# Optimization experiments

Measured on AMD Instinct MI355X. Metric: run time of the kernel, lower is better.

The kernel has to match this reference:

```python
import jax, jax.numpy as jnp
import numpy as np

N_NODES = 50000
N_EDGES = 800000
IN_C, HID_C, OUT_C = 256, 256, 64


def _glorot(key, shape):
    fan_in, fan_out = shape[1], shape[0]
    lim = float(np.sqrt(6.0 / (fan_in + fan_out)))
    return jax.random.uniform(key, shape, jnp.float32, -lim, lim)


def setup_inputs() -> dict:
    key = jax.random.key(0)
    ks = jax.random.split(key, 8)
    x = jax.random.normal(ks[0], (N_NODES, IN_C), jnp.float32)
    edge_index = jax.random.randint(ks[1], (2, N_EDGES), 0, N_NODES, jnp.int64)
    # layer 1: SAGEConv(IN_C -> HID_C): lin_l (agg neighbors, has bias), lin_r (root, no bias)
    W_l1 = _glorot(ks[2], (HID_C, IN_C))
    b1 = jnp.zeros((HID_C,), jnp.float32)
    W_r1 = _glorot(ks[3], (HID_C, IN_C))
    # layer 2: SAGEConv(HID_C -> OUT_C)
    W_l2 = _glorot(ks[4], (OUT_C, HID_C))
    b2 = jnp.zeros((OUT_C,), jnp.float32)
    W_r2 = _glorot(ks[5], (OUT_C, HID_C))
    return {"x": x, "W_l1": W_l1, "b1": b1, "W_r1": W_r1,
            "W_l2": W_l2, "b2": b2, "W_r2": W_r2, "edge_index": edge_index}


def _sage_conv(x, src, dst, W_l, b, W_r, n_nodes):
    # mean aggregation of source-node features into destination nodes
    msg = x[src]                                               # [E, C]
    agg = jax.ops.segment_sum(msg, dst, num_segments=n_nodes)  # [N, C]
    deg = jax.ops.segment_sum(jnp.ones((src.shape[0],), x.dtype), dst,
                              num_segments=n_nodes)            # [N]
    agg = agg / jnp.maximum(deg, 1.0)[:, None]
    # out = lin_l(agg) + lin_r(x); bias only on lin_l (PyG SAGEConv default)
    return agg @ W_l.T + b + x @ W_r.T


def reference(x, W_l1, b1, W_r1, W_l2, b2, W_r2, edge_index):
    src, dst = edge_index[0], edge_index[1]
    n = x.shape[0]
    h = _sage_conv(x, src, dst, W_l1, b1, W_r1, n)
    h = jax.nn.relu(h)  # dropout is identity in eval mode
    out = _sage_conv(h, src, dst, W_l2, b2, W_r2, n)
    return out
```

## Files before the change

### kernel.cpp

```cpp
#include <hip/hip_runtime.h>

#define IN_C 256
#define HID_C 256
#define OUT_C 64

#define NBK 64
#define NPAD 50176
#define N2 (NPAD / 2)
#define NCH (NPAD / 256)

typedef __attribute__((ext_vector_type(8))) short bf16x8;
typedef __attribute__((ext_vector_type(4))) float f32x4;
typedef __attribute__((ext_vector_type(2))) float f32x2;
typedef __attribute__((ext_vector_type(8))) unsigned short ushortx8;
typedef __attribute__((ext_vector_type(4))) unsigned int u32x4;
typedef __attribute__((ext_vector_type(2))) unsigned int u32x2;

__device__ inline float b2f(unsigned short u) {
    union { unsigned int u; float f; } v; v.u = ((unsigned int)u) << 16; return v.f;
}
__device__ inline unsigned short f2b(float f) {
    union { float f; unsigned int u; } v; v.f = f;
    unsigned int u = v.u;
    unsigned int r = (u + 0x7fffu + ((u >> 16) & 1u)) >> 16;
    return (unsigned short)r;
}

__device__ __forceinline__ unsigned char f2fp8(float v) {
    int pk = __builtin_amdgcn_cvt_pk_fp8_f32(v, v, 0, false);
    return (unsigned char)(pk & 0xff);
}
__device__ __forceinline__ void fp8acc4(unsigned int w, float& a0, float& a1, float& a2, float& a3) {
    f32x2 lo = __builtin_amdgcn_cvt_pk_f32_fp8((int)w, false);
    f32x2 hi = __builtin_amdgcn_cvt_pk_f32_fp8((int)w, true);
    a0 += lo.x; a1 += lo.y; a2 += hi.x; a3 += hi.y;
}

__device__ __forceinline__ void gl2lds16(const ushort* g, ushort* l) {
    __builtin_amdgcn_global_load_lds((const __attribute__((address_space(1))) void*)g,
                                     (__attribute__((address_space(3))) void*)l, 16, 0, 0);
}

__device__ __forceinline__ void conv8(const float* __restrict__ src, ushort* __restrict__ dst, int u) {
    const float4* p = (const float4*)(src + (size_t)u * 8);
    float4 a = p[0], b = p[1];
    ushort4 o0 = make_ushort4(f2b(a.x), f2b(a.y), f2b(a.z), f2b(a.w));
    ushort4 o1 = make_ushort4(f2b(b.x), f2b(b.y), f2b(b.z), f2b(b.w));
    ((ushort4*)(dst + (size_t)u * 8))[0] = o0;
    ((ushort4*)(dst + (size_t)u * 8))[1] = o1;
}


__global__ __launch_bounds__(1024) void k_front(const int* __restrict__ dst, int E, int EPB,
                                                ushort* __restrict__ rank,
                                                unsigned int* __restrict__ cnt32,
                                                int* __restrict__ chunkpart,
                                                const float* __restrict__ Wl1, const float* __restrict__ Wr1,
                                                const float* __restrict__ Wl2, const float* __restrict__ Wr2,
                                                ushort* __restrict__ Wc1, ushort* __restrict__ Wc2) {
    const int bid = blockIdx.x;
    const int t = threadIdx.x;

    if (bid < NBK) {
        __shared__ unsigned int h[N2];
        for (int i = t; i < N2; i += 1024) h[i] = 0;
        __syncthreads();

        const int e0 = bid * EPB;
        const int e1 = min(e0 + EPB, E);
        for (int e = e0 + t; e < e1; e += 1024) {
            int d = dst[e];
            int sh = (d & 1) << 4;
            unsigned int old = atomicAdd(&h[d >> 1], 1u << sh);
            rank[e] = (ushort)((old >> sh) & 0xffffu);
        }
        __syncthreads();

        unsigned int* outp = cnt32 + (size_t)bid * N2;
        for (int i = t; i < N2; i += 1024) outp[i] = h[i];

        if (t < NCH) {
            int c = t;
            int sum = 0;
#pragma unroll 8
            for (int j = 0; j < 128; ++j) {
                unsigned int v = h[c * 128 + ((j + c) & 127)];
                sum += (int)(v & 0xffffu) + (int)(v >> 16);
            }
            chunkpart[c * NBK + bid] = sum;
        }
        return;
    }

    const int i = (bid - NBK) * 1024 + t;
    if (i < 20480) {
        if (i < 8192)       conv8(Wl1, Wc1,         i);
        else if (i < 16384) conv8(Wr1, Wc1 + 65536, i - 8192);
        else if (i < 18432) conv8(Wl2, Wc2,         i - 16384);
        else                conv8(Wr2, Wc2 + 16384, i - 18432);
    }
}


__global__ __launch_bounds__(256) void k_scan(const unsigned int* __restrict__ cnt32,
                                              const int* __restrict__ chunkpart, int N,
                                              int* __restrict__ row_start,
                                              ushort* __restrict__ off16) {
    __shared__ int s[256];
    const int bid = blockIdx.x;
    const int t = threadIdx.x;

    int pre = 0;
    const int limit = bid * NBK;
    for (int i = t; i < limit; i += 256) pre += chunkpart[i];
    s[t] = pre;
    __syncthreads();
    for (int o = 128; o > 0; o >>= 1) {
        if (t < o) s[t] += s[t + o];
        __syncthreads();
    }
    const int chunk_off = s[0];
    __syncthreads();

    const int i = bid * 256 + t;
    const ushort* cnt16 = (const ushort*)cnt32;
    int run = 0;
#pragma unroll 8
    for (int b = 0; b < NBK; ++b) {
        ushort cv = cnt16[(size_t)b * NPAD + i];
        off16[(size_t)b * NPAD + i] = (ushort)run;
        run += cv;
    }
    int deg = run;

    s[t] = deg;
    __syncthreads();
    for (int o = 1; o < 256; o <<= 1) {
        int xx = (t >= o) ? s[t - o] : 0;
        __syncthreads();
        s[t] += xx;
        __syncthreads();
    }
    if (i < N) row_start[i + 1] = s[t] + chunk_off;
    if (i == 0) row_start[0] = 0;
}


__global__ __launch_bounds__(256) void k_gemm_l1(const float* __restrict__ x,
                                                 const ushort* __restrict__ W,
                                                 unsigned char* __restrict__ Cp,
                                                 ushort* __restrict__ Cr,
                                                 int N, int nScat,
                                                 const int* __restrict__ src, const int* __restrict__ dst,
                                                 const ushort* __restrict__ rank,
                                                 const int* __restrict__ row_start,
                                                 const ushort* __restrict__ off16,
                                                 int E, int EPB, int per, int* __restrict__ eidx) {
    if (blockIdx.x < (unsigned)nScat) {
        const int e0 = blockIdx.x * per;
        const int e1 = min(e0 + per, E);
        for (int e = e0 + (int)threadIdx.x; e < e1; e += 256) {
            int d = dst[e];
            int b = e / EPB;
            eidx[row_start[d] + (int)off16[(size_t)b * NPAD + d] + (int)rank[e]] = src[e];
        }
        return;
    }

    __shared__ ushort Aall[64 * 256];
    __shared__ ushort Wb[2 * 128 * 64];

    const int bx = blockIdx.x - nScat;
    const int t = threadIdx.x;
    const int bm = bx * 64;

    const int wid  = t >> 6;
    const int lane = t & 63;
    const int wr = wid >> 1;
    const int wc = wid & 1;
    const int lr = lane & 15;
    const int lk = lane >> 4;

    {
        const int r4  = t >> 2;
        const int cg  = t & 3;
        const int row = bm + r4;
        const float4* xp = (const float4*)(x + (size_t)row * 256 + cg * 64);
        float4 v[16];
        if (row < N) {
#pragma unroll
            for (int j = 0; j < 16; ++j) v[j] = xp[j];
        } else {
#pragma unroll
            for (int j = 0; j < 16; ++j) v[j] = make_float4(0.f, 0.f, 0.f, 0.f);
        }
        const int r7 = r4 & 7;
#pragma unroll
        for (int j = 0; j < 8; ++j) {
            float4 a = v[2 * j], b = v[2 * j + 1];
            ushort4 o0 = make_ushort4(f2b(a.x), f2b(a.y), f2b(a.z), f2b(a.w));
            ushort4 o1 = make_ushort4(f2b(b.x), f2b(b.y), f2b(b.z), f2b(b.w));
            ushort* dp = Aall + r4 * 256 + (cg * 8 + (j ^ r7)) * 8;
            ((ushort4*)dp)[0] = o0;
            ((ushort4*)dp)[1] = o1;
        }
        const int wrow7 = (t >> 3) & 7;
        const int wsrc  = ((t & 7) ^ wrow7) << 3;
#pragma unroll
        for (int i = 0; i < 4; ++i) {
            gl2lds16(W + (size_t)(i * 32 + (t >> 3)) * 256 + 0 + wsrc,
                     Wb + i * 2048 + t * 8);
        }
    }
    __syncthreads();

    f32x4 acc[2][4];
    int s = 0;
#pragma unroll
    for (int by = 0; by < 4; ++by) {
#pragma unroll
        for (int m = 0; m < 2; ++m)
#pragma unroll
            for (int n = 0; n < 4; ++n) acc[m][n] = (f32x4){0.f, 0.f, 0.f, 0.f};

#pragma unroll
        for (int kk = 0; kk < 4; ++kk, ++s) {
            const int sn = s + 1;
            if (sn < 16) {
                const int by_n = sn >> 2, kk_n = sn & 3, buf_n = sn & 1;
                const int wrow7 = (t >> 3) & 7;
                const int wsrc  = ((t & 7) ^ wrow7) << 3;
#pragma unroll
                for (int i = 0; i < 4; ++i) {
                    gl2lds16(W + (size_t)(by_n * 128 + i * 32 + (t >> 3)) * 256 + kk_n * 64 + wsrc,
                             Wb + buf_n * 8192 + i * 2048 + t * 8);
                }
            }

            const int kb = kk * 8;
            const int buf = s & 1;
            const int sw = lr & 7;
#pragma unroll
            for (int ks = 0; ks < 2; ++ks) {
                bf16x8 a[2], b[4];
                const int ck = ks * 4 + lk;
#pragma unroll
                for (int m = 0; m < 2; ++m)
                    a[m] = *(const bf16x8*)(Aall + (wr * 32 + m * 16 + lr) * 256 + ((kb + (ck ^ sw)) << 3));
#pragma unroll
                for (int n = 0; n < 4; ++n)
                    b[n] = *(const bf16x8*)(Wb + buf * 8192 + (wc * 64 + n * 16 + lr) * 64 + ((ck ^ sw) << 3));
#pragma unroll
                for (int m = 0; m < 2; ++m)
#pragma unroll
                    for (int n = 0; n < 4; ++n)
                        acc[m][n] = __builtin_amdgcn_mfma_f32_16x16x32_bf16(a[m], b[n], acc[m][n], 0, 0, 0);
            }

            if (kk == 3) {
                const bool isP = (by * 128 + wc * 64) < HID_C;
#pragma unroll
                for (int m = 0; m < 2; ++m)
#pragma unroll
                    for (int r2 = 0; r2 < 4; ++r2) {
                        int row = bm + wr * 32 + m * 16 + lk * 4 + r2;
                        if (row < N) {
                            if (isP) {
#pragma unroll
                                for (int n = 0; n < 4; ++n) {
                                    int col = by * 128 + wc * 64 + n * 16 + lr;
                                    Cp[(size_t)row * HID_C + col] = f2fp8(acc[m][n][r2]);
                                }
                            } else {
#pragma unroll
                                for (int n = 0; n < 4; ++n) {
                                    int col = by * 128 + wc * 64 + n * 16 + lr - HID_C;
                                    Cr[(size_t)row * HID_C + col] = f2b(acc[m][n][r2]);
                                }
                            }
                        }
                    }
            }
            __syncthreads();
        }
    }
}


__global__ __launch_bounds__(256) void k_gemm_mfma(const ushort* __restrict__ A,
                                                   const ushort* __restrict__ W,
                                                   unsigned char* __restrict__ Cp,
                                                   ushort* __restrict__ Cr,
                                                   int N, int K, int PC, int nby, int nwg) {
    __shared__ ushort As[2][128 * 64];
    __shared__ ushort Bs[2][128 * 64];

    const int orig = blockIdx.x;
    const int q = nwg >> 3, r = nwg & 7;
    const int xcd = orig & 7;
    const int base = (xcd < r) ? xcd * (q + 1) : r * (q + 1) + (xcd - r) * q;
    const int wgid = base + (orig >> 3);
    const int bx = wgid / nby, by = wgid % nby;

    const int wid  = threadIdx.x >> 6;
    const int lane = threadIdx.x & 63;
    const int wr = wid >> 1, wc = wid & 1;
    const int bm = bx * 128;
    const int bn = by * 128;
    const int lr = lane & 15;
    const int lk = lane >> 4;
    const int srow   = lane >> 3;
    const int schunk = lane & 7;

    f32x4 acc[4][4];
#pragma unroll
    for (int m = 0; m < 4; ++m)
#pragma unroll
        for (int n = 0; n < 4; ++n) acc[m][n] = (f32x4){0.f, 0.f, 0.f, 0.f};

#pragma unroll
    for (int i = 0; i < 4; ++i) {
        int seg = wid * 4 + i;
        int row = seg * 8 + srow;
        gl2lds16(A + (size_t)(bm + row) * K + schunk * 8, As[0] + seg * 512);
        gl2lds16(W + (size_t)(bn + row) * K + schunk * 8, Bs[0] + seg * 512);
    }
    __syncthreads();

    int cur = 0;
    for (int k0 = 0; k0 < K; k0 += 64) {
        const int kn = k0 + 64;
        if (kn < K) {
#pragma unroll
            for (int i = 0; i < 4; ++i) {
                int seg = wid * 4 + i;
                int row = seg * 8 + srow;
                gl2lds16(A + (size_t)(bm + row) * K + kn + schunk * 8, As[cur ^ 1] + seg * 512);
                gl2lds16(W + (size_t)(bn + row) * K + kn + schunk * 8, Bs[cur ^ 1] + seg * 512);
            }
        }

#pragma unroll
        for (int ks = 0; ks < 2; ++ks) {
            bf16x8 a[4], b[4];
#pragma unroll
            for (int m = 0; m < 4; ++m)
                a[m] = *(const bf16x8*)(As[cur] + (wr * 64 + m * 16 + lr) * 64 + ks * 32 + lk * 8);
#pragma unroll
            for (int n = 0; n < 4; ++n)
                b[n] = *(const bf16x8*)(Bs[cur] + (wc * 64 + n * 16 + lr) * 64 + ks * 32 + lk * 8);
#pragma unroll
            for (int m = 0; m < 4; ++m)
#pragma unroll
                for (int n = 0; n < 4; ++n)
                    acc[m][n] = __builtin_amdgcn_mfma_f32_16x16x32_bf16(a[m], b[n], acc[m][n], 0, 0, 0);
        }
        __syncthreads();
        cur ^= 1;
    }

    const bool isP = (bn + wc * 64) < PC;
#pragma unroll
    for (int m = 0; m < 4; ++m)
#pragma unroll
        for (int r2 = 0; r2 < 4; ++r2) {
            int row = bm + wr * 64 + m * 16 + lk * 4 + r2;
            if (row < N) {
                if (isP) {
#pragma unroll
                    for (int n = 0; n < 4; ++n) {
                        int col = bn + wc * 64 + n * 16 + lr;
                        Cp[(size_t)row * PC + col] = f2fp8(acc[m][n][r2]);
                    }
                } else {
#pragma unroll
                    for (int n = 0; n < 4; ++n) {
                        int col = bn + wc * 64 + n * 16 + lr - PC;
                        Cr[(size_t)row * PC + col] = f2b(acc[m][n][r2]);
                    }
                }
            }
        }
}


__global__ __launch_bounds__(256) void k_agg1(const unsigned char* __restrict__ P1,
                                              const ushort* __restrict__ R1,
                                              const float* __restrict__ bias,
                                              const int* __restrict__ row_start,
                                              const int* __restrict__ eidx,
                                              ushort* __restrict__ h, int N) {
    int node = (blockIdx.x * blockDim.x + threadIdx.x) >> 6;
    int lane = threadIdx.x & 63;
    if (node >= N) return;
    const int slot = lane >> 4;
    const int sub  = lane & 15;
    int s0 = row_start[node], s1 = row_start[node + 1];

    float acc[16];
#pragma unroll
    for (int i = 0; i < 16; ++i) acc[i] = 0.f;

    for (int e = s0 + slot; e < s1; e += 16) {
        int e1 = e + 4, e2 = e + 8, e3 = e + 12;
        bool h1 = e1 < s1, h2 = e2 < s1, h3 = e3 < s1;
        int sA = eidx[e];
        int sB = h1 ? eidx[e1] : sA;
        int sC = h2 ? eidx[e2] : sA;
        int sD = h3 ? eidx[e3] : sA;
        u32x4 a = *(const u32x4*)(P1 + (size_t)sA * 256 + sub * 16);
        u32x4 b = *(const u32x4*)(P1 + (size_t)sB * 256 + sub * 16);
        u32x4 c = *(const u32x4*)(P1 + (size_t)sC * 256 + sub * 16);
        u32x4 d = *(const u32x4*)(P1 + (size_t)sD * 256 + sub * 16);
#pragma unroll
        for (int w = 0; w < 4; ++w) fp8acc4(a[w], acc[w*4], acc[w*4+1], acc[w*4+2], acc[w*4+3]);
        if (h1) {
#pragma unroll
            for (int w = 0; w < 4; ++w) fp8acc4(b[w], acc[w*4], acc[w*4+1], acc[w*4+2], acc[w*4+3]);
        }
        if (h2) {
#pragma unroll
            for (int w = 0; w < 4; ++w) fp8acc4(c[w], acc[w*4], acc[w*4+1], acc[w*4+2], acc[w*4+3]);
        }
        if (h3) {
#pragma unroll
            for (int w = 0; w < 4; ++w) fp8acc4(d[w], acc[w*4], acc[w*4+1], acc[w*4+2], acc[w*4+3]);
        }
    }

#pragma unroll
    for (int i = 0; i < 16; ++i) {
        acc[i] += __shfl_xor(acc[i], 16, 64);
        acc[i] += __shfl_xor(acc[i], 32, 64);
    }

    if (slot == 0) {
        int d = s1 - s0;
        float inv = 1.0f / (float)(d > 1 ? d : 1);
        const ushort* rp = R1 + (size_t)node * 256 + sub * 16;
        ushortx8 r0 = *(const ushortx8*)(rp);
        ushortx8 r1 = *(const ushortx8*)(rp + 8);
        const float* bp = bias + sub * 16;
        ushortx8 o0, o1;
#pragma unroll
        for (int i = 0; i < 8; ++i) {
            float v0 = fmaxf(acc[i] * inv + bp[i] + b2f(r0[i]), 0.f);
            float v1 = fmaxf(acc[i + 8] * inv + bp[i + 8] + b2f(r1[i]), 0.f);
            o0[i] = f2b(v0);
            o1[i] = f2b(v1);
        }
        ushort* hp = h + (size_t)node * 256 + sub * 16;
        *(ushortx8*)(hp) = o0;
        *(ushortx8*)(hp + 8) = o1;
    }
}


__global__ __launch_bounds__(256) void k_agg2(const unsigned char* __restrict__ P2,
                                              const ushort* __restrict__ R2,
                                              const float* __restrict__ bias,
                                              const int* __restrict__ row_start,
                                              const int* __restrict__ eidx,
                                              float* __restrict__ out, int N) {
    int node = (blockIdx.x * blockDim.x + threadIdx.x) >> 6;
    int lane = threadIdx.x & 63;
    if (node >= N) return;
    const int slot = lane >> 3;
    const int sub  = lane & 7;
    int s0 = row_start[node], s1 = row_start[node + 1];

    float acc[8];
#pragma unroll
    for (int i = 0; i < 8; ++i) acc[i] = 0.f;

    for (int e = s0 + slot; e < s1; e += 32) {
        int e1 = e + 8, e2 = e + 16, e3 = e + 24;
        bool h1 = e1 < s1, h2 = e2 < s1, h3 = e3 < s1;
        int sA = eidx[e];
        int sB = h1 ? eidx[e1] : sA;
        int sC = h2 ? eidx[e2] : sA;
        int sD = h3 ? eidx[e3] : sA;
        u32x2 a = *(const u32x2*)(P2 + (size_t)sA * 64 + sub * 8);
        u32x2 b = *(const u32x2*)(P2 + (size_t)sB * 64 + sub * 8);
        u32x2 c = *(const u32x2*)(P2 + (size_t)sC * 64 + sub * 8);
        u32x2 d = *(const u32x2*)(P2 + (size_t)sD * 64 + sub * 8);
#pragma unroll
        for (int w = 0; w < 2; ++w) fp8acc4(a[w], acc[w*4], acc[w*4+1], acc[w*4+2], acc[w*4+3]);
        if (h1) {
#pragma unroll
            for (int w = 0; w < 2; ++w) fp8acc4(b[w], acc[w*4], acc[w*4+1], acc[w*4+2], acc[w*4+3]);
        }
        if (h2) {
#pragma unroll
            for (int w = 0; w < 2; ++w) fp8acc4(c[w], acc[w*4], acc[w*4+1], acc[w*4+2], acc[w*4+3]);
        }
        if (h3) {
#pragma unroll
            for (int w = 0; w < 2; ++w) fp8acc4(d[w], acc[w*4], acc[w*4+1], acc[w*4+2], acc[w*4+3]);
        }
    }

#pragma unroll
    for (int i = 0; i < 8; ++i) {
        acc[i] += __shfl_xor(acc[i], 8, 64);
        acc[i] += __shfl_xor(acc[i], 16, 64);
        acc[i] += __shfl_xor(acc[i], 32, 64);
    }

    if (slot == 0) {
        int d = s1 - s0;
        float inv = 1.0f / (float)(d > 1 ? d : 1);
        ushortx8 rv = *(const ushortx8*)(R2 + (size_t)node * 64 + sub * 8);
        const float* bp = bias + sub * 8;
        float o[8];
#pragma unroll
        for (int i = 0; i < 8; ++i) o[i] = acc[i] * inv + bp[i] + b2f(rv[i]);
        float4* op = (float4*)(out + (size_t)node * 64 + sub * 8);
        op[0] = make_float4(o[0], o[1], o[2], o[3]);
        op[1] = make_float4(o[4], o[5], o[6], o[7]);
    }
}


extern "C" void kernel_launch(void* const* d_in, const int* in_sizes, int n_in,
                              void* d_out, int out_size, void* d_ws, size_t ws_size,
                              hipStream_t stream) {
    const float* x    = (const float*)d_in[0];
    const float* W_l1 = (const float*)d_in[1];
    const float* b1   = (const float*)d_in[2];
    const float* W_r1 = (const float*)d_in[3];
    const float* W_l2 = (const float*)d_in[4];
    const float* b2   = (const float*)d_in[5];
    const float* W_r2 = (const float*)d_in[6];
    const int*   ei   = (const int*)d_in[7];

    const int N = in_sizes[0] / IN_C;
    const int E = in_sizes[7] / 2;
    const int EPB = (E + NBK - 1) / NBK;
    const int* src = ei;
    const int* dst = ei + E;

    char* ws = (char*)d_ws;
    size_t off_ = 0;
    auto alloc = [&](size_t bytes) -> void* {
        void* p = ws + off_;
        off_ += (bytes + 255) & ~(size_t)255;
        return p;
    };
    unsigned int*  cnt32     = (unsigned int*)alloc((size_t)NBK * N2 * 4);
    ushort*        off16     = (ushort*)alloc((size_t)NBK * NPAD * 2);
    int*           chunkpart = (int*)alloc((size_t)NCH * NBK * 4);
    int*           row_start = (int*)alloc((size_t)(N + 1) * 4);
    ushort*        rank      = (ushort*)alloc((size_t)E * 2);
    int*           eidx      = (int*)alloc((size_t)E * 4);
    ushort*        Wc1       = (ushort*)alloc((size_t)2 * HID_C * IN_C * 2);
    ushort*        Wc2       = (ushort*)alloc((size_t)2 * OUT_C * HID_C * 2);
    unsigned char* P1        = (unsigned char*)alloc((size_t)N * HID_C);
    ushort*        R1        = (ushort*)alloc((size_t)N * HID_C * 2);
    ushort*        h         = (ushort*)alloc((size_t)N * HID_C * 2);
    unsigned char* P2        = (unsigned char*)alloc((size_t)N * OUT_C);
    ushort*        R2        = (ushort*)alloc((size_t)N * OUT_C * 2);
    (void)alloc(128 * 512 * 2);
    (void)ws_size; (void)n_in; (void)out_size;

    k_front<<<NBK + 32, 1024, 0, stream>>>(dst, E, EPB, rank, cnt32, chunkpart,
                                           W_l1, W_r1, W_l2, W_r2, Wc1, Wc2);

    k_scan<<<NCH, 256, 0, stream>>>(cnt32, chunkpart, N, row_start, off16);

    {
        const int nScat = 448;
        const int per = (E + nScat - 1) / nScat;
        const int nbx = (N + 63) / 64;
        k_gemm_l1<<<nScat + nbx, 256, 0, stream>>>(x, Wc1, P1, R1, N, nScat,
                                                   src, dst, rank, row_start, off16,
                                                   E, EPB, per, eidx);
        k_agg1<<<(N + 3) / 4, 256, 0, stream>>>(P1, R1, b1, row_start, eidx, h, N);
    }

    {
        int nbx = (N + 127) / 128, nby = (2 * OUT_C) / 128;
        int nwg = nbx * nby;
        k_gemm_mfma<<<nwg, 256, 0, stream>>>(h, Wc2, P2, R2, N, HID_C, OUT_C, nby, nwg);
        k_agg2<<<(N + 3) / 4, 256, 0, stream>>>(P2, R2, b2, row_start, eidx, (float*)d_out, N);
    }
}
```

Measured before the change: 148.3 us.

## Load GEMM weights directly from global memory and split layer-1 columns across workgroups

```diff
diff --git a/kernel.cpp b/kernel.cpp
--- a/kernel.cpp
+++ b/kernel.cpp
@@ -168,18 +168,13 @@
     }
 
     __shared__ ushort Aall[64 * 256];
-    __shared__ ushort Wb[2 * 128 * 64];
-
-    const int bx = blockIdx.x - nScat;
+
+    const int orig = blockIdx.x - nScat;
+    const int wgid = (orig & 7) * 196 + (orig >> 3);
+    const int bx = wgid >> 1, by = wgid & 1;
+    const int bm = bx * 64;
+
     const int t = threadIdx.x;
-    const int bm = bx * 64;
-
-    const int wid  = t >> 6;
-    const int lane = t & 63;
-    const int wr = wid >> 1;
-    const int wc = wid & 1;
-    const int lr = lane & 15;
-    const int lk = lane >> 4;
 
     {
         const int r4  = t >> 2;
@@ -204,179 +199,137 @@
             ((ushort4*)dp)[0] = o0;
             ((ushort4*)dp)[1] = o1;
         }
-        const int wrow7 = (t >> 3) & 7;
-        const int wsrc  = ((t & 7) ^ wrow7) << 3;
-#pragma unroll
-        for (int i = 0; i < 4; ++i) {
-            gl2lds16(W + (size_t)(i * 32 + (t >> 3)) * 256 + 0 + wsrc,
-                     Wb + i * 2048 + t * 8);
-        }
     }
     __syncthreads();
 
-    f32x4 acc[2][4];
-    int s = 0;
-#pragma unroll
-    for (int by = 0; by < 4; ++by) {
-#pragma unroll
-        for (int m = 0; m < 2; ++m)
-#pragma unroll
-            for (int n = 0; n < 4; ++n) acc[m][n] = (f32x4){0.f, 0.f, 0.f, 0.f};
-
-#pragma unroll
-        for (int kk = 0; kk < 4; ++kk, ++s) {
-            const int sn = s + 1;
-            if (sn < 16) {
-                const int by_n = sn >> 2, kk_n = sn & 3, buf_n = sn & 1;
-                const int wrow7 = (t >> 3) & 7;
-                const int wsrc  = ((t & 7) ^ wrow7) << 3;
-#pragma unroll
-                for (int i = 0; i < 4; ++i) {
-                    gl2lds16(W + (size_t)(by_n * 128 + i * 32 + (t >> 3)) * 256 + kk_n * 64 + wsrc,
-                             Wb + buf_n * 8192 + i * 2048 + t * 8);
+    const int wid = t >> 6, lane = t & 63;
+    const int lr = lane & 15, lk = lane >> 4;
+    const int cb = by * 256 + wid * 64;
+    const bool isP = cb < HID_C;
+    const int sw = lr & 7;
+    const ushort* wp0 = W + (size_t)(cb + lr) * 256 + lk * 8;
+
+    f32x4 acc[4][4];
+#pragma unroll
+    for (int m = 0; m < 4; ++m)
+#pragma unroll
+        for (int n = 0; n < 4; ++n) acc[m][n] = (f32x4){0.f, 0.f, 0.f, 0.f};
+
+#pragma unroll
+    for (int kk = 0; kk < 4; ++kk) {
+#pragma unroll
+        for (int ks = 0; ks < 2; ++ks) {
+            const int ck = ks * 4 + lk;
+            bf16x8 a[4], b[4];
+#pragma unroll
+            for (int n = 0; n < 4; ++n)
+                b[n] = *(const bf16x8*)(wp0 + (size_t)n * 16 * 256 + kk * 64 + ks * 32);
+#pragma unroll
+            for (int m = 0; m < 4; ++m)
+                a[m] = *(const bf16x8*)(Aall + (m * 16 + lr) * 256 + ((kk * 8 + (ck ^ sw)) << 3));
+#pragma unroll
+            for (int m = 0; m < 4; ++m)
+#pragma unroll
+                for (int n = 0; n < 4; ++n)
+                    acc[m][n] = __builtin_amdgcn_mfma_f32_16x16x32_bf16(a[m], b[n], acc[m][n], 0, 0, 0);
+        }
+    }
+
+#pragma unroll
+    for (int m = 0; m < 4; ++m)
+#pragma unroll
+        for (int r2 = 0; r2 < 4; ++r2) {
+            int row = bm + m * 16 + lk * 4 + r2;
+            if (row < N) {
+                if (isP) {
+#pragma unroll
+                    for (int n = 0; n < 4; ++n) {
+                        int col = cb + n * 16 + lr;
+                        Cp[(size_t)row * HID_C + col] = f2fp8(acc[m][n][r2]);
+                    }
+                } else {
+#pragma unroll
+                    for (int n = 0; n < 4; ++n) {
+                        int col = cb + n * 16 + lr - HID_C;
+                        Cr[(size_t)row * HID_C + col] = f2b(acc[m][n][r2]);
+                    }
                 }
             }
-
-            const int kb = kk * 8;
-            const int buf = s & 1;
-            const int sw = lr & 7;
-#pragma unroll
-            for (int ks = 0; ks < 2; ++ks) {
-                bf16x8 a[2], b[4];
-                const int ck = ks * 4 + lk;
-#pragma unroll
-                for (int m = 0; m < 2; ++m)
-                    a[m] = *(const bf16x8*)(Aall + (wr * 32 + m * 16 + lr) * 256 + ((kb + (ck ^ sw)) << 3));
-#pragma unroll
-                for (int n = 0; n < 4; ++n)
-                    b[n] = *(const bf16x8*)(Wb + buf * 8192 + (wc * 64 + n * 16 + lr) * 64 + ((ck ^ sw) << 3));
-#pragma unroll
-                for (int m = 0; m < 2; ++m)
-#pragma unroll
-                    for (int n = 0; n < 4; ++n)
-                        acc[m][n] = __builtin_amdgcn_mfma_f32_16x16x32_bf16(a[m], b[n], acc[m][n], 0, 0, 0);
-            }
-
-            if (kk == 3) {
-                const bool isP = (by * 128 + wc * 64) < HID_C;
-#pragma unroll
-                for (int m = 0; m < 2; ++m)
-#pragma unroll
-                    for (int r2 = 0; r2 < 4; ++r2) {
-                        int row = bm + wr * 32 + m * 16 + lk * 4 + r2;
-                        if (row < N) {
-                            if (isP) {
-#pragma unroll
-                                for (int n = 0; n < 4; ++n) {
-                                    int col = by * 128 + wc * 64 + n * 16 + lr;
-                                    Cp[(size_t)row * HID_C + col] = f2fp8(acc[m][n][r2]);
-                                }
-                            } else {
-#pragma unroll
-                                for (int n = 0; n < 4; ++n) {
-                                    int col = by * 128 + wc * 64 + n * 16 + lr - HID_C;
-                                    Cr[(size_t)row * HID_C + col] = f2b(acc[m][n][r2]);
-                                }
-                            }
-                        }
-                    }
-            }
-            __syncthreads();
-        }
-    }
-}
-
-
-__global__ __launch_bounds__(256) void k_gemm_mfma(const ushort* __restrict__ A,
-                                                   const ushort* __restrict__ W,
-                                                   unsigned char* __restrict__ Cp,
-                                                   ushort* __restrict__ Cr,
-                                                   int N, int K, int PC, int nby, int nwg) {
-    __shared__ ushort As[2][128 * 64];
-    __shared__ ushort Bs[2][128 * 64];
+        }
+}
+
+
+__global__ __launch_bounds__(256) void k_gemm_l2(const ushort* __restrict__ A,
+                                                 const ushort* __restrict__ W,
+                                                 unsigned char* __restrict__ Cp,
+                                                 ushort* __restrict__ Cr,
+                                                 int N) {
+    __shared__ ushort Aall[64 * 256];
 
     const int orig = blockIdx.x;
-    const int q = nwg >> 3, r = nwg & 7;
-    const int xcd = orig & 7;
-    const int base = (xcd < r) ? xcd * (q + 1) : r * (q + 1) + (xcd - r) * q;
-    const int wgid = base + (orig >> 3);
-    const int bx = wgid / nby, by = wgid % nby;
-
-    const int wid  = threadIdx.x >> 6;
-    const int lane = threadIdx.x & 63;
-    const int wr = wid >> 1, wc = wid & 1;
-    const int bm = bx * 128;
-    const int bn = by * 128;
-    const int lr = lane & 15;
-    const int lk = lane >> 4;
-    const int srow   = lane >> 3;
-    const int schunk = lane & 7;
-
-    f32x4 acc[4][4];
+    const int bx = (orig & 7) * 98 + (orig >> 3);
+    const int bm = bx * 64;
+    const int t = threadIdx.x;
+
+    {
+        const int arow7 = (t >> 5) & 7;
+        const int asrc  = ((t & 31) ^ arow7) << 3;
+#pragma unroll
+        for (int i = 0; i < 8; ++i)
+            gl2lds16(A + (size_t)(bm + i * 8 + (t >> 5)) * 256 + asrc, Aall + i * 2048 + t * 8);
+    }
+    __syncthreads();
+
+    const int wid = t >> 6, lane = t & 63;
+    const int lr = lane & 15, lk = lane >> 4;
+    const int cb = wid * 32;
+    const bool isP = cb < OUT_C;
+    const int sw = lr & 7;
+    const ushort* wp0 = W + (size_t)(cb + lr) * 256 + lk * 8;
+
+    f32x4 acc[4][2];
 #pragma unroll
     for (int m = 0; m < 4; ++m)
 #pragma unroll
-        for (int n = 0; n < 4; ++n) acc[m][n] = (f32x4){0.f, 0.f, 0.f, 0.f};
-
-#pragma unroll
-    for (int i = 0; i < 4; ++i) {
-        int seg = wid * 4 + i;
-        int row = seg * 8 + srow;
-        gl2lds16(A + (size_t)(bm + row) * K + schunk * 8, As[0] + seg * 512);
-        gl2lds16(W + (size_t)(bn + row) * K + schunk * 8, Bs[0] + seg * 512);
-    }
-    __syncthreads();
-
-    int cur = 0;
-    for (int k0 = 0; k0 < K; k0 += 64) {
-        const int kn = k0 + 64;
-        if (kn < K) {
-#pragma unroll
-            for (int i = 0; i < 4; ++i) {
-                int seg = wid * 4 + i;
-                int row = seg * 8 + srow;
-                gl2lds16(A + (size_t)(bm + row) * K + kn + schunk * 8, As[cur ^ 1] + seg * 512);
-                gl2lds16(W + (size_t)(bn + row) * K + kn + schunk * 8, Bs[cur ^ 1] + seg * 512);
-            }
-        }
-
+        for (int n = 0; n < 2; ++n) acc[m][n] = (f32x4){0.f, 0.f, 0.f, 0.f};
+
+#pragma unroll
+    for (int kk = 0; kk < 4; ++kk) {
 #pragma unroll
         for (int ks = 0; ks < 2; ++ks) {
-            bf16x8 a[4], b[4];
+            const int ck = ks * 4 + lk;
+            bf16x8 a[4], b[2];
+#pragma unroll
+            for (int n = 0; n < 2; ++n)
+                b[n] = *(const bf16x8*)(wp0 + (size_t)n * 16 * 256 + kk * 64 + ks * 32);
 #pragma unroll
             for (int m = 0; m < 4; ++m)
-                a[m] = *(const bf16x8*)(As[cur] + (wr * 64 + m * 16 + lr) * 64 + ks * 32 + lk * 8);
-#pragma unroll
-            for (int n = 0; n < 4; ++n)
-                b[n] = *(const bf16x8*)(Bs[cur] + (wc * 64 + n * 16 + lr) * 64 + ks * 32 + lk * 8);
+                a[m] = *(const bf16x8*)(Aall + (m * 16 + lr) * 256 + ((kk * 8 + (ck ^ sw)) << 3));
 #pragma unroll
             for (int m = 0; m < 4; ++m)
 #pragma unroll
-                for (int n = 0; n < 4; ++n)
+                for (int n = 0; n < 2; ++n)
                     acc[m][n] = __builtin_amdgcn_mfma_f32_16x16x32_bf16(a[m], b[n], acc[m][n], 0, 0, 0);
         }
-        __syncthreads();
-        cur ^= 1;
-    }
-
-    const bool isP = (bn + wc * 64) < PC;
+    }
+
 #pragma unroll
     for (int m = 0; m < 4; ++m)
 #pragma unroll
         for (int r2 = 0; r2 < 4; ++r2) {
-            int row = bm + wr * 64 + m * 16 + lk * 4 + r2;
+            int row = bm + m * 16 + lk * 4 + r2;
             if (row < N) {
                 if (isP) {
 #pragma unroll
-                    for (int n = 0; n < 4; ++n) {
-                        int col = bn + wc * 64 + n * 16 + lr;
-                        Cp[(size_t)row * PC + col] = f2fp8(acc[m][n][r2]);
+                    for (int n = 0; n < 2; ++n) {
+                        int col = cb + n * 16 + lr;
+                        Cp[(size_t)row * OUT_C + col] = f2fp8(acc[m][n][r2]);
                     }
                 } else {
 #pragma unroll
-                    for (int n = 0; n < 4; ++n) {
-                        int col = bn + wc * 64 + n * 16 + lr - PC;
-                        Cr[(size_t)row * PC + col] = f2b(acc[m][n][r2]);
+                    for (int n = 0; n < 2; ++n) {
+                        int col = cb + n * 16 + lr - OUT_C;
+                        Cr[(size_t)row * OUT_C + col] = f2b(acc[m][n][r2]);
                     }
                 }
             }
@@ -571,17 +524,16 @@
     {
         const int nScat = 448;
         const int per = (E + nScat - 1) / nScat;
-        const int nbx = (N + 63) / 64;
-        k_gemm_l1<<<nScat + nbx, 256, 0, stream>>>(x, Wc1, P1, R1, N, nScat,
+        const int nwg = 2 * (NPAD / 64);
+        k_gemm_l1<<<nScat + nwg, 256, 0, stream>>>(x, Wc1, P1, R1, N, nScat,
                                                    src, dst, rank, row_start, off16,
                                                    E, EPB, per, eidx);
         k_agg1<<<(N + 3) / 4, 256, 0, stream>>>(P1, R1, b1, row_start, eidx, h, N);
     }
 
     {
-        int nbx = (N + 127) / 128, nby = (2 * OUT_C) / 128;
-        int nwg = nbx * nby;
-        k_gemm_mfma<<<nwg, 256, 0, stream>>>(h, Wc2, P2, R2, N, HID_C, OUT_C, nby, nwg);
+        const int nwg = NPAD / 64;
+        k_gemm_l2<<<nwg, 256, 0, stream>>>(h, Wc2, P2, R2, N);
         k_agg2<<<(N + 3) / 4, 256, 0, stream>>>(P2, R2, b2, row_start, eidx, (float*)d_out, N);
     }
 }
```

New measurement: 161.1 us. +8.6%, slower.
